# Kernel optimization log

Measured on AMD Instinct MI355X. Metric: run time of the kernel, lower is better.

## Reference

```python
import jax, jax.numpy as jnp
import numpy as np

NPERSEG = 1024
NOVERLAP = 768
STEP = NPERSEG - NOVERLAP  # 256
BATCH = 1024
SEQ_LEN = 16384


def setup_inputs() -> dict:
    key = jax.random.key(0)
    k1, k2, k3, k4 = jax.random.split(key, 4)
    inp = jax.random.normal(k1, (BATCH, SEQ_LEN), dtype=jnp.float32)
    freqs = jax.random.uniform(k2, (NPERSEG,), dtype=jnp.float32)  # learned freq params
    fc_w = jax.random.normal(k3, (1, 1), dtype=jnp.float32)
    fc_b = jax.random.normal(k4, (1,), dtype=jnp.float32)
    return {"input": inp, "freqs": freqs, "fc_w": fc_w, "fc_b": fc_b}


def reference(input, freqs, fc_w, fc_b):
    B, S = input.shape
    nwin = (S - NPERSEG) // STEP + 1  # number of overlapping windows
    # gather all windows at once: [nwin, NPERSEG] index grid
    idx = jnp.arange(nwin)[:, None] * STEP + jnp.arange(NPERSEG)[None, :]
    win = input[:, idx]  # [B, nwin, NPERSEG]
    # complex weights v = exp(-2*pi*i*freqs), applied as real/imag parts
    ang = (2.0 * jnp.pi) * freqs
    re = jnp.einsum('bwp,p->bw', win, jnp.cos(ang))   # Re(x . v)
    im = jnp.einsum('bwp,p->bw', win, -jnp.sin(ang))  # Im(x . v)
    # mean over windows, then |.|^2
    fr = jnp.mean(re, axis=1)
    fi = jnp.mean(im, axis=1)
    psd = (fr * fr + fi * fi)[:, None]  # [B, 1]
    # Linear(1,1)
    return psd @ fc_w.T + fc_b
```

## Files before the change

### kernel.cpp

```cpp
#include <hip/hip_runtime.h>
#include <math.h>

#define NPERSEG 1024
#define STEP    256
#define NWIN    61
#define SEQ     16384
#define BATCH   1024

typedef float f32x4 __attribute__((ext_vector_type(4)));

__global__ __launch_bounds__(256, 4) void welch_fused_kernel(
        const float* __restrict__ inp,
        const float* __restrict__ freqs,
        const float* __restrict__ fc_w,
        const float* __restrict__ fc_b,
        float* __restrict__ out) {
    const int row = blockIdx.x;
    const int t   = threadIdx.x;

    float Fc[4], Fs[4], Pc[4], Ps[4], Sc[4], Ss[4];
    #pragma unroll
    for (int e = 0; e < 4; ++e) {
        int idx = 4 * t + e;
        int p0  = idx & 255;
        int q   = idx >> 8;
        float fc_ = 0.f, fs_ = 0.f, pc_ = 0.f, ps_ = 0.f, sc_ = 0.f, ss_ = 0.f;
        #pragma unroll
        for (int k = 0; k < 4; ++k) {
            float a = 6.2831853071795864769f * freqs[p0 + 256 * k];
            float sv, cv;
            sincosf(a, &sv, &cv);
            cv *= (1.0f / NWIN);
            sv *= -(1.0f / NWIN);
            fc_ += cv; fs_ += sv;
            if (k <= q) { pc_ += cv; ps_ += sv; }
            if (k >= q) { sc_ += cv; ss_ += sv; }
        }
        Fc[e] = fc_; Fs[e] = fs_;
        Pc[e] = pc_; Ps[e] = ps_;
        Sc[e] = sc_; Ss[e] = ss_;
    }

    const f32x4* __restrict__ x4 = (const f32x4*)(inp + (size_t)row * SEQ);

    float sr = 0.f, si = 0.f;
    {
        f32x4 x = x4[t];
        sr += x.x * Pc[0] + x.y * Pc[1] + x.z * Pc[2] + x.w * Pc[3];
        si += x.x * Ps[0] + x.y * Ps[1] + x.z * Ps[2] + x.w * Ps[3];
    }
    #pragma unroll 7
    for (int i = 1; i < 15; ++i) {
        f32x4 x = x4[t + 256 * i];
        sr += x.x * Fc[0] + x.y * Fc[1] + x.z * Fc[2] + x.w * Fc[3];
        si += x.x * Fs[0] + x.y * Fs[1] + x.z * Fs[2] + x.w * Fs[3];
    }
    {
        f32x4 x = x4[t + 256 * 15];
        sr += x.x * Sc[0] + x.y * Sc[1] + x.z * Sc[2] + x.w * Sc[3];
        si += x.x * Ss[0] + x.y * Ss[1] + x.z * Ss[2] + x.w * Ss[3];
    }

    #pragma unroll
    for (int off = 32; off > 0; off >>= 1) {
        sr += __shfl_down(sr, off, 64);
        si += __shfl_down(si, off, 64);
    }

    __shared__ float red[4][2];
    int wave = t >> 6;
    int lane = t & 63;
    if (lane == 0) { red[wave][0] = sr; red[wave][1] = si; }
    __syncthreads();

    if (t == 0) {
        float fr = red[0][0] + red[1][0] + red[2][0] + red[3][0];
        float fi = red[0][1] + red[1][1] + red[2][1] + red[3][1];
        out[row] = (fr * fr + fi * fi) * fc_w[0] + fc_b[0];
    }
}

extern "C" void kernel_launch(void* const* d_in, const int* in_sizes, int n_in,
                              void* d_out, int out_size, void* d_ws, size_t ws_size,
                              hipStream_t stream) {
    const float* inp   = (const float*)d_in[0];
    const float* freqs = (const float*)d_in[1];
    const float* fc_w  = (const float*)d_in[2];
    const float* fc_b  = (const float*)d_in[3];
    float* out = (float*)d_out;

    welch_fused_kernel<<<BATCH, 256, 0, stream>>>(inp, freqs, fc_w, fc_b, out);
}
```

Baseline: 98.02 us.

## Precompute folded sincos weights in a prologue kernel and batch all row loads

```diff
diff --git a/kernel.cpp b/kernel.cpp
--- a/kernel.cpp
+++ b/kernel.cpp
@@ -9,57 +9,64 @@
 
 typedef float f32x4 __attribute__((ext_vector_type(4)));
 
+__global__ __launch_bounds__(256) void welch_weights_kernel(
+        const float* __restrict__ freqs,
+        float* __restrict__ W) {
+    const int idx = blockIdx.x * 256 + threadIdx.x;
+    const int p0  = idx & 255;
+    const int q   = idx >> 8;
+    float fc_ = 0.f, fs_ = 0.f, pc_ = 0.f, ps_ = 0.f, sc_ = 0.f, ss_ = 0.f;
+    #pragma unroll
+    for (int k = 0; k < 4; ++k) {
+        float a = 6.2831853071795864769f * freqs[p0 + 256 * k];
+        float sv, cv;
+        sincosf(a, &sv, &cv);
+        cv *= (1.0f / NWIN);
+        sv *= -(1.0f / NWIN);
+        fc_ += cv; fs_ += sv;
+        if (k <= q) { pc_ += cv; ps_ += sv; }
+        if (k >= q) { sc_ += cv; ss_ += sv; }
+    }
+    W[0 * 1024 + idx] = fc_;
+    W[1 * 1024 + idx] = fs_;
+    W[2 * 1024 + idx] = pc_;
+    W[3 * 1024 + idx] = ps_;
+    W[4 * 1024 + idx] = sc_;
+    W[5 * 1024 + idx] = ss_;
+}
+
 __global__ __launch_bounds__(256, 4) void welch_fused_kernel(
         const float* __restrict__ inp,
-        const float* __restrict__ freqs,
+        const float* __restrict__ W,
         const float* __restrict__ fc_w,
         const float* __restrict__ fc_b,
         float* __restrict__ out) {
     const int row = blockIdx.x;
     const int t   = threadIdx.x;
 
-    float Fc[4], Fs[4], Pc[4], Ps[4], Sc[4], Ss[4];
-    #pragma unroll
-    for (int e = 0; e < 4; ++e) {
-        int idx = 4 * t + e;
-        int p0  = idx & 255;
-        int q   = idx >> 8;
-        float fc_ = 0.f, fs_ = 0.f, pc_ = 0.f, ps_ = 0.f, sc_ = 0.f, ss_ = 0.f;
-        #pragma unroll
-        for (int k = 0; k < 4; ++k) {
-            float a = 6.2831853071795864769f * freqs[p0 + 256 * k];
-            float sv, cv;
-            sincosf(a, &sv, &cv);
-            cv *= (1.0f / NWIN);
-            sv *= -(1.0f / NWIN);
-            fc_ += cv; fs_ += sv;
-            if (k <= q) { pc_ += cv; ps_ += sv; }
-            if (k >= q) { sc_ += cv; ss_ += sv; }
-        }
-        Fc[e] = fc_; Fs[e] = fs_;
-        Pc[e] = pc_; Ps[e] = ps_;
-        Sc[e] = sc_; Ss[e] = ss_;
-    }
+    const f32x4* __restrict__ W4 = (const f32x4*)W;
+    f32x4 Fc = W4[0 * 256 + t];
+    f32x4 Fs = W4[1 * 256 + t];
+    f32x4 Pc = W4[2 * 256 + t];
+    f32x4 Ps = W4[3 * 256 + t];
+    f32x4 Sc = W4[4 * 256 + t];
+    f32x4 Ss = W4[5 * 256 + t];
 
     const f32x4* __restrict__ x4 = (const f32x4*)(inp + (size_t)row * SEQ);
 
-    float sr = 0.f, si = 0.f;
-    {
-        f32x4 x = x4[t];
-        sr += x.x * Pc[0] + x.y * Pc[1] + x.z * Pc[2] + x.w * Pc[3];
-        si += x.x * Ps[0] + x.y * Ps[1] + x.z * Ps[2] + x.w * Ps[3];
+    f32x4 X[16];
+    #pragma unroll
+    for (int i = 0; i < 16; ++i) X[i] = x4[t + 256 * i];
+
+    float sr = X[0].x * Pc.x + X[0].y * Pc.y + X[0].z * Pc.z + X[0].w * Pc.w;
+    float si = X[0].x * Ps.x + X[0].y * Ps.y + X[0].z * Ps.z + X[0].w * Ps.w;
+    #pragma unroll
+    for (int i = 1; i < 15; ++i) {
+        sr += X[i].x * Fc.x + X[i].y * Fc.y + X[i].z * Fc.z + X[i].w * Fc.w;
+        si += X[i].x * Fs.x + X[i].y * Fs.y + X[i].z * Fs.z + X[i].w * Fs.w;
     }
-    #pragma unroll 7
-    for (int i = 1; i < 15; ++i) {
-        f32x4 x = x4[t + 256 * i];
-        sr += x.x * Fc[0] + x.y * Fc[1] + x.z * Fc[2] + x.w * Fc[3];
-        si += x.x * Fs[0] + x.y * Fs[1] + x.z * Fs[2] + x.w * Fs[3];
-    }
-    {
-        f32x4 x = x4[t + 256 * 15];
-        sr += x.x * Sc[0] + x.y * Sc[1] + x.z * Sc[2] + x.w * Sc[3];
-        si += x.x * Ss[0] + x.y * Ss[1] + x.z * Ss[2] + x.w * Ss[3];
-    }
+    sr += X[15].x * Sc.x + X[15].y * Sc.y + X[15].z * Sc.z + X[15].w * Sc.w;
+    si += X[15].x * Ss.x + X[15].y * Ss.y + X[15].z * Ss.z + X[15].w * Ss.w;
 
     #pragma unroll
     for (int off = 32; off > 0; off >>= 1) {
@@ -68,8 +75,8 @@
     }
 
     __shared__ float red[4][2];
-    int wave = t >> 6;
-    int lane = t & 63;
+    const int wave = t >> 6;
+    const int lane = t & 63;
     if (lane == 0) { red[wave][0] = sr; red[wave][1] = si; }
     __syncthreads();
 
@@ -88,6 +95,8 @@
     const float* fc_w  = (const float*)d_in[2];
     const float* fc_b  = (const float*)d_in[3];
     float* out = (float*)d_out;
+    float* W   = (float*)d_ws;
 
-    welch_fused_kernel<<<BATCH, 256, 0, stream>>>(inp, freqs, fc_w, fc_b, out);
+    welch_weights_kernel<<<4, 256, 0, stream>>>(freqs, W);
+    welch_fused_kernel<<<BATCH, 256, 0, stream>>>(inp, W, fc_w, fc_b, out);
 }
```

New measurement: 95.82 us. -2.2%, faster.

## Prefetch all row data into registers and share sincos via LDS

Applied to the files above, without the earlier changes.

```diff
diff --git a/kernel.cpp b/kernel.cpp
--- a/kernel.cpp
+++ b/kernel.cpp
@@ -8,6 +8,7 @@
 #define BATCH   1024
 
 typedef float f32x4 __attribute__((ext_vector_type(4)));
+typedef float f32x2 __attribute__((ext_vector_type(2)));
 
 __global__ __launch_bounds__(256, 4) void welch_fused_kernel(
         const float* __restrict__ inp,
@@ -18,48 +19,56 @@
     const int row = blockIdx.x;
     const int t   = threadIdx.x;
 
+    const f32x4* __restrict__ x4 = (const f32x4*)(inp + (size_t)row * SEQ);
+
+    f32x4 X[16];
+    #pragma unroll
+    for (int i = 0; i < 16; ++i) X[i] = x4[t + 256 * i];
+
+    __shared__ f32x2 cs[NPERSEG];
+    {
+        f32x4 f = ((const f32x4*)freqs)[t];
+        #pragma unroll
+        for (int e = 0; e < 4; ++e) {
+            float a = 6.2831853071795864769f * f[e];
+            float sv, cv;
+            sincosf(a, &sv, &cv);
+            f32x2 v;
+            v.x = cv * (1.0f / NWIN);
+            v.y = sv * (-(1.0f / NWIN));
+            cs[4 * t + e] = v;
+        }
+    }
+    __syncthreads();
+
     float Fc[4], Fs[4], Pc[4], Ps[4], Sc[4], Ss[4];
     #pragma unroll
     for (int e = 0; e < 4; ++e) {
-        int idx = 4 * t + e;
-        int p0  = idx & 255;
-        int q   = idx >> 8;
+        const int idx = 4 * t + e;
+        const int p0  = idx & 255;
+        const int q   = idx >> 8;
         float fc_ = 0.f, fs_ = 0.f, pc_ = 0.f, ps_ = 0.f, sc_ = 0.f, ss_ = 0.f;
         #pragma unroll
         for (int k = 0; k < 4; ++k) {
-            float a = 6.2831853071795864769f * freqs[p0 + 256 * k];
-            float sv, cv;
-            sincosf(a, &sv, &cv);
-            cv *= (1.0f / NWIN);
-            sv *= -(1.0f / NWIN);
-            fc_ += cv; fs_ += sv;
-            if (k <= q) { pc_ += cv; ps_ += sv; }
-            if (k >= q) { sc_ += cv; ss_ += sv; }
+            f32x2 v = cs[p0 + 256 * k];
+            fc_ += v.x; fs_ += v.y;
+            if (k <= q) { pc_ += v.x; ps_ += v.y; }
+            if (k >= q) { sc_ += v.x; ss_ += v.y; }
         }
         Fc[e] = fc_; Fs[e] = fs_;
         Pc[e] = pc_; Ps[e] = ps_;
         Sc[e] = sc_; Ss[e] = ss_;
     }
 
-    const f32x4* __restrict__ x4 = (const f32x4*)(inp + (size_t)row * SEQ);
-
-    float sr = 0.f, si = 0.f;
-    {
-        f32x4 x = x4[t];
-        sr += x.x * Pc[0] + x.y * Pc[1] + x.z * Pc[2] + x.w * Pc[3];
-        si += x.x * Ps[0] + x.y * Ps[1] + x.z * Ps[2] + x.w * Ps[3];
+    float sr = X[0].x * Pc[0] + X[0].y * Pc[1] + X[0].z * Pc[2] + X[0].w * Pc[3];
+    float si = X[0].x * Ps[0] + X[0].y * Ps[1] + X[0].z * Ps[2] + X[0].w * Ps[3];
+    #pragma unroll
+    for (int i = 1; i < 15; ++i) {
+        sr += X[i].x * Fc[0] + X[i].y * Fc[1] + X[i].z * Fc[2] + X[i].w * Fc[3];
+        si += X[i].x * Fs[0] + X[i].y * Fs[1] + X[i].z * Fs[2] + X[i].w * Fs[3];
     }
-    #pragma unroll 7
-    for (int i = 1; i < 15; ++i) {
-        f32x4 x = x4[t + 256 * i];
-        sr += x.x * Fc[0] + x.y * Fc[1] + x.z * Fc[2] + x.w * Fc[3];
-        si += x.x * Fs[0] + x.y * Fs[1] + x.z * Fs[2] + x.w * Fs[3];
-    }
-    {
-        f32x4 x = x4[t + 256 * 15];
-        sr += x.x * Sc[0] + x.y * Sc[1] + x.z * Sc[2] + x.w * Sc[3];
-        si += x.x * Ss[0] + x.y * Ss[1] + x.z * Ss[2] + x.w * Ss[3];
-    }
+    sr += X[15].x * Sc[0] + X[15].y * Sc[1] + X[15].z * Sc[2] + X[15].w * Sc[3];
+    si += X[15].x * Ss[0] + X[15].y * Ss[1] + X[15].z * Ss[2] + X[15].w * Ss[3];
 
     #pragma unroll
     for (int off = 32; off > 0; off >>= 1) {
@@ -68,8 +77,8 @@
     }
 
     __shared__ float red[4][2];
-    int wave = t >> 6;
-    int lane = t & 63;
+    const int wave = t >> 6;
+    const int lane = t & 63;
     if (lane == 0) { red[wave][0] = sr; red[wave][1] = si; }
     __syncthreads();
 
```

Result: faster. 92.79 us (-5.3%).
